# Optimization experiments

Measured on AMD Instinct MI355X. Metric: run time of the kernel, lower is better.

## Reference

```python
import jax, jax.numpy as jnp
from jax import lax
import numpy as np

N, C_IN, C_OUT, H, W, D = 16, 32, 64, 128, 128, 5


def setup_inputs() -> dict:
    key = jax.random.key(0)
    k1, k2, k3, k4 = jax.random.split(key, 4)
    x = jax.random.normal(k1, (N, 1, C_IN, H, W), jnp.float32)
    d = jax.random.normal(k2, (N, C_OUT, C_IN, D, D), jnp.float32)
    y = jax.random.normal(k3, (N, C_OUT, 1, H, W), jnp.float32)
    alpha = jax.random.uniform(k4, (N, 1, 1, 1), jnp.float32)
    return {"x": x, "d": d, "y": y, "alpha": alpha, "reg": 1.0}


def _cross_corr(wts, img, pad):
    # out[i, j, u, v] = sum_{h,w} wts[i,h,w] * img[j, h+u-pad, w+v-pad]
    # (valid sums, zero padding). Implements the per-sample full-image conv3d
    # of the torch code (cross-correlation, no kernel flip).
    out = lax.conv_general_dilated(img[:, None], wts[:, None], (1, 1),
                                   [(pad, pad), (pad, pad)])
    return out.transpose(1, 0, 2, 3)  # (Ci_wts, Cj_img, 2*pad+1, 2*pad+1)


def reference(x, d, y, alpha, reg):
    n, _, c_in, h, w = x.shape
    c_out, ds = d.shape[1], d.shape[-1]
    K = c_in * ds * ds
    # Full autocorrelation R[n,c0,c1,a,b] = sum x[c0,h,w]*x[c1,h+a-(ds-1), w+b-(ds-1)]
    R = jax.vmap(lambda xn: _cross_corr(xn, xn, ds - 1))(x[:, 0])  # (n,C,C,2ds-1,2ds-1)
    # Toeplitz block assembly: Q[(c0,p,q),(c1,s,t)] = R[c0,c1, s-p+ds-1, t-q+ds-1]
    shift = jnp.arange(ds)[None, :] - jnp.arange(ds)[:, None] + (ds - 1)  # [p,s]
    Qa = R[:, :, :, shift, :]            # (n,c0,c1,p,s,2ds-1)
    Qb = Qa[..., shift]                  # (n,c0,c1,p,s,q,t)
    Q = Qb.transpose(0, 1, 3, 5, 2, 4, 6).reshape(n, K, K)
    # X^T y: S[n,o,c,u,v] = sum y[o,h,w]*x[c, h+u-p0, w+v-p0], p0=(ds-1)//2
    S = jax.vmap(lambda yn, xn: _cross_corr(yn, xn, (ds - 1) // 2))(y[:, :, 0], x[:, 0])
    P = S.transpose(0, 2, 3, 4, 1).reshape(n, K, c_out)
    # Tikhonov regularization around previous dictionary d
    a = alpha.reshape(n, 1) * (h * w * reg / (ds * ds * c_in))  # (n,1)
    Q = Q + a[:, :, None] * jnp.eye(K, dtype=Q.dtype)
    P = P + a[:, :, None] * d.reshape(n, c_out, K).transpose(0, 2, 1)
    # Batched Cholesky solve: D = Q^{-1} P
    L = jnp.linalg.cholesky(Q)
    z = lax.linalg.triangular_solve(L, P, left_side=True, lower=True)
    Dsol = lax.linalg.triangular_solve(L, z, left_side=True, lower=True, transpose_a=True)
    return Dsol.reshape(n, c_in, ds, ds, c_out).transpose(0, 4, 1, 2, 3)
```

## Files before the change

kernel.cpp:

```cpp
#include <hip/hip_runtime.h>

#define R_SZ    737280
#define Q_SZ    10240000
#define P_SZ    819200
#define LI_SZ   1024000
#define W_SZ    4608000

typedef unsigned short u16;
typedef __attribute__((ext_vector_type(8))) short bf16x8;
typedef __attribute__((ext_vector_type(4))) float f32x4;

#define MFMA16(a, b, c) __builtin_amdgcn_mfma_f32_16x16x32_bf16(a, b, c, 0, 0, 0)

__device__ __forceinline__ float alpha_scale(const float* alpha, const float* reg, int n) {
  return alpha[n] * (16384.0f * reg[0] / 800.0f);
}

__device__ __forceinline__ u16 f2bf(float f) {
  union { float f; unsigned u; } v; v.f = f;
  unsigned r = v.u + 0x7FFFu + ((v.u >> 16) & 1u);
  return (u16)(r >> 16);
}
__device__ __forceinline__ float bf2f(u16 h) {
  union { unsigned u; float f; } v; v.u = ((unsigned)h) << 16; return v.f;
}

__device__ __forceinline__ bf16x8 load8(const u16* p) {
  union { uint4 d; bf16x8 v; } u;
  u.d = *(const uint4*)p;
  return u.v;
}

__device__ __forceinline__ bf16x8 build_frag(const unsigned* w, int s) {
  union { unsigned u[4]; bf16x8 v; } f;
  int b = s >> 1;
  if (s & 1) {
    #pragma unroll
    for (int k = 0; k < 4; ++k) f.u[k] = (w[b + k] >> 16) | (w[b + k + 1] << 16);
  } else {
    #pragma unroll
    for (int k = 0; k < 4; ++k) f.u[k] = w[b + k];
  }
  return f.v;
}

__device__ __forceinline__ void stage_row(u16* slot, int partStride,
                                          const float* __restrict__ img,
                                          int C, int r, bool valid,
                                          int tid, int nthr) {
  for (int idx = tid; idx < C * 16; idx += nthr) {
    int c = idx >> 4, m = idx & 15;
    float v[8];
    if (valid) {
      const float* p = img + ((size_t)c * 128 + r) * 128 + m * 8;
      float4 a = *(const float4*)p;
      float4 b = *(const float4*)(p + 4);
      v[0]=a.x; v[1]=a.y; v[2]=a.z; v[3]=a.w; v[4]=b.x; v[5]=b.y; v[6]=b.z; v[7]=b.w;
    } else {
      #pragma unroll
      for (int k = 0; k < 8; ++k) v[k] = 0.0f;
    }
    union { u16 s[8]; uint2 d[2]; } hh, ll;
    #pragma unroll
    for (int k = 0; k < 8; ++k) {
      u16 h = f2bf(v[k]);
      hh.s[k] = h;
      ll.s[k] = f2bf(v[k] - bf2f(h));
    }
    u16* dh = slot + c * 136 + 4 + m * 8;
    *(uint2*)(dh)     = hh.d[0];
    *(uint2*)(dh + 4) = hh.d[1];
    u16* dl = dh + partStride;
    *(uint2*)(dl)     = ll.d[0];
    *(uint2*)(dl + 4) = ll.d[1];
  }
}

#define SLOT_US 8704
#define PSTR_32 4352
#define YPSTR   8704

__global__ __launch_bounds__(640) void k_corrR_mfma(const float* __restrict__ x,
                                                    float* __restrict__ Rpart) {
  __shared__ __align__(16) u16 lds[5 * SLOT_US];
  int n  = blockIdx.x >> 4;
  int r0 = (blockIdx.x & 15) << 3;
  int tid = threadIdx.x;
  const float* xn = x + (size_t)n * 32 * 128 * 128;

  if (tid < 320) {
    int s = tid / 64, p = (tid >> 5) & 1, c = tid & 31;
    u16* b = lds + s * SLOT_US + p * PSTR_32 + c * 136;
    uint2 z; z.x = 0; z.y = 0;
    *(uint2*)b = z;
    *(uint2*)(b + 132) = z;
  }
  for (int rr = 0; rr < 5; ++rr) {
    int r = r0 + rr;
    stage_row(lds + (r % 5) * SLOT_US, PSTR_32, xn, 32, r, r < 128, tid, 640);
  }

  int wave = tid >> 6, lane = tid & 63;
  int du = wave >> 1, nt = wave & 1;
  int lm = lane & 15, q = lane >> 4;

  f32x4 acc[9][2];
  #pragma unroll
  for (int dvi = 0; dvi < 9; ++dvi)
    #pragma unroll
    for (int mt = 0; mt < 2; ++mt) acc[dvi][mt] = (f32x4){0.f, 0.f, 0.f, 0.f};

  for (int i = r0; i < r0 + 8; ++i) {
    __syncthreads();
    const u16* A  = lds + (i % 5) * SLOT_US;
    const u16* Bp = lds + ((i + du) % 5) * SLOT_US;
    #pragma unroll
    for (int ks = 0; ks < 4; ++ks) {
      int kb = ks * 32 + q * 8;
      bf16x8 af[2][2];
      #pragma unroll
      for (int pa = 0; pa < 2; ++pa)
        #pragma unroll
        for (int mt = 0; mt < 2; ++mt)
          af[pa][mt] = load8(A + pa * PSTR_32 + (mt * 16 + lm) * 136 + 4 + kb);
      #pragma unroll
      for (int pb = 0; pb < 2; ++pb) {
        const u16* wp = Bp + pb * PSTR_32 + (nt * 16 + lm) * 136 + kb;
        uint4 w0 = *(const uint4*)wp;
        uint4 w1 = *(const uint4*)(wp + 8);
        unsigned w[8] = {w0.x, w0.y, w0.z, w0.w, w1.x, w1.y, w1.z, w1.w};
        #pragma unroll
        for (int dvi = 0; dvi < 9; ++dvi) {
          bf16x8 bf = build_frag(w, dvi);
          #pragma unroll
          for (int mt = 0; mt < 2; ++mt)
            #pragma unroll
            for (int pa = 0; pa < 2; ++pa) {
              if (pa == 1 && pb == 1) continue;
              acc[dvi][mt] = MFMA16(af[pa][mt], bf, acc[dvi][mt]);
            }
        }
      }
    }
    __syncthreads();
    if (i + 1 < r0 + 8) {
      int r = i + 5;
      stage_row(lds + (r % 5) * SLOT_US, PSTR_32, xn, 32, r, r < 128, tid, 640);
    }
  }

  float* Rp = Rpart + (size_t)blockIdx.x * 46080;
  #pragma unroll
  for (int dvi = 0; dvi < 9; ++dvi)
    #pragma unroll
    for (int mt = 0; mt < 2; ++mt) {
      float* dst = Rp + (du * 9 + dvi) * 1024 + (nt * 16 + lm) * 32 + mt * 16 + q * 4;
      *(f32x4*)dst = acc[dvi][mt];
    }
}

__global__ void k_reduceR(const float* __restrict__ part, float* __restrict__ R) {
  int idx = blockIdx.x * 256 + threadIdx.x;
  int n = idx / 46080, rem = idx % 46080;
  const float* p = part + (size_t)n * 16 * 46080 + rem;
  float s = 0.0f;
  #pragma unroll
  for (int c = 0; c < 16; ++c) s += p[(size_t)c * 46080];
  R[idx] = s;
}

__global__ __launch_bounds__(640) void k_corrP_mfma(const float* __restrict__ x,
                                                    const float* __restrict__ y,
                                                    float* __restrict__ Ppart) {
  __shared__ __align__(16) u16 xs[5 * SLOT_US];
  __shared__ __align__(16) u16 ys[2 * YPSTR];
  int n  = blockIdx.x >> 4;
  int r0 = (blockIdx.x & 15) << 3;
  int tid = threadIdx.x;
  const float* xn = x + (size_t)n * 32 * 128 * 128;
  const float* yn = y + (size_t)n * 64 * 128 * 128;

  if (tid < 320) {
    int s = tid / 64, p = (tid >> 5) & 1, c = tid & 31;
    u16* b = xs + s * SLOT_US + p * PSTR_32 + c * 136;
    uint2 z; z.x = 0; z.y = 0;
    *(uint2*)b = z;
    *(uint2*)(b + 132) = z;
  }
  for (int rr = -2; rr <= 2; ++rr) {
    int r = r0 + rr;
    stage_row(xs + ((r + 10) % 5) * SLOT_US, PSTR_32, xn, 32, r,
              (r >= 0 && r < 128), tid, 640);
  }
  stage_row(ys, YPSTR, yn, 64, r0, true, tid, 640);

  int wave = tid >> 6, lane = tid & 63;
  int du = (wave >> 1) - 2, mh = wave & 1;
  int lm = lane & 15, q = lane >> 4;

  f32x4 acc[5][2][2];
  #pragma unroll
  for (int dvi = 0; dvi < 5; ++dvi)
    #pragma unroll
    for (int mt = 0; mt < 2; ++mt)
      #pragma unroll
      for (int nt = 0; nt < 2; ++nt)
        acc[dvi][mt][nt] = (f32x4){0.f, 0.f, 0.f, 0.f};

  for (int i = r0; i < r0 + 8; ++i) {
    __syncthreads();
    const u16* Bp = xs + ((i + du + 10) % 5) * SLOT_US;
    #pragma unroll
    for (int ks = 0; ks < 4; ++ks) {
      int kb = ks * 32 + q * 8;
      bf16x8 af[2][2];
      #pragma unroll
      for (int pa = 0; pa < 2; ++pa)
        #pragma unroll
        for (int mt = 0; mt < 2; ++mt)
          af[pa][mt] = load8(ys + pa * YPSTR + (mh * 32 + mt * 16 + lm) * 136 + 4 + kb);
      #pragma unroll
      for (int nt = 0; nt < 2; ++nt)
        #pragma unroll
        for (int pb = 0; pb < 2; ++pb) {
          const u16* wp = Bp + pb * PSTR_32 + (nt * 16 + lm) * 136 + kb;
          uint4 w0 = *(const uint4*)wp;
          uint4 w1 = *(const uint4*)(wp + 8);
          unsigned w[8] = {w0.x, w0.y, w0.z, w0.w, w1.x, w1.y, w1.z, w1.w};
          #pragma unroll
          for (int dvi = 0; dvi < 5; ++dvi) {
            bf16x8 bf = build_frag(w, dvi + 2);
            #pragma unroll
            for (int mt = 0; mt < 2; ++mt)
              #pragma unroll
              for (int pa = 0; pa < 2; ++pa) {
                if (pa == 1 && pb == 1) continue;
                acc[dvi][mt][nt] = MFMA16(af[pa][mt], bf, acc[dvi][mt][nt]);
              }
          }
        }
    }
    __syncthreads();
    if (i + 1 < r0 + 8) {
      int r = i + 3;
      stage_row(xs + ((r + 10) % 5) * SLOT_US, PSTR_32, xn, 32, r,
                (r >= 0 && r < 128), tid, 640);
      stage_row(ys, YPSTR, yn, 64, i + 1, true, tid, 640);
    }
  }

  float* Pp = Ppart + (size_t)blockIdx.x * 51200;
  #pragma unroll
  for (int dvi = 0; dvi < 5; ++dvi)
    #pragma unroll
    for (int mt = 0; mt < 2; ++mt)
      #pragma unroll
      for (int nt = 0; nt < 2; ++nt) {
        float* dst = Pp + ((du + 2) * 5 + dvi) * 2048 + (nt * 16 + lm) * 64
                        + mh * 32 + mt * 16 + q * 4;
        *(f32x4*)dst = acc[dvi][mt][nt];
      }
}

__global__ void k_reduceP(const float* __restrict__ part, const float* __restrict__ d,
                          const float* __restrict__ alpha, const float* __restrict__ reg,
                          float* __restrict__ P) {
  int idx = blockIdx.x * 256 + threadIdx.x;
  int n = idx / 51200, rem = idx % 51200;
  int k = rem >> 6, co = rem & 63;
  int ci = k / 25, ae = k % 25;
  const float* p = part + (size_t)n * 16 * 51200 + (ae * 32 + ci) * 64 + co;
  float s = 0.0f;
  #pragma unroll
  for (int c = 0; c < 16; ++c) s += p[(size_t)c * 51200];
  float a = alpha_scale(alpha, reg, n);
  P[idx] = s + a * d[((size_t)n * 64 + co) * 800 + k];
}

__global__ void k_buildQ(const float* __restrict__ R, float* __restrict__ Q,
                         const float* __restrict__ alpha, const float* __restrict__ reg) {
  int bid = blockIdx.x;
  int n = bid / 800, k1 = bid % 800;
  int c1 = k1 / 25, r1 = k1 % 25, a = r1 / 5, e = r1 % 5;
  float av = alpha_scale(alpha, reg, n);
  const float* Rn = R + (size_t)n * 45 * 1024;
  float* Qrow = Q + ((size_t)n * 800 + k1) * 800;
  for (int k2 = threadIdx.x; k2 < 800; k2 += 256) {
    int c2 = k2 / 25, r2 = k2 % 25, b = r2 / 5, f = r2 % 5;
    int du = b - a, dv = f - e;
    float v = (du >= 0)
      ? Rn[(du * 9 + dv + 4) * 1024 + c2 * 32 + c1]
      : Rn[((-du) * 9 + 4 - dv) * 1024 + c1 * 32 + c2];
    if (k2 == k1) v += av;
    Qrow[k2] = v;
  }
}

#define DS 82

__device__ void diag_factor_invert2(float* As, float* Bs,
                                    float* __restrict__ Ln, float* __restrict__ LnT,
                                    int tid) {
  __shared__ float Dinv_s[16 * 25];
  for (int s = 0; s < 16; ++s) {
    int b = 5 * s;
    float a[5][5], dinv[5];
    #pragma unroll
    for (int ii = 0; ii < 5; ++ii)
      #pragma unroll
      for (int kk = 0; kk <= ii; ++kk) a[ii][kk] = As[(b+ii)*DS + b+kk];
    #pragma unroll
    for (int jj = 0; jj < 5; ++jj) {
      float dd = sqrtf(a[jj][jj]);
      a[jj][jj] = dd; dinv[jj] = 1.0f / dd;
      #pragma unroll
      for (int ii = jj+1; ii < 5; ++ii) a[ii][jj] *= dinv[jj];
      #pragma unroll
      for (int ii = jj+1; ii < 5; ++ii)
        #pragma unroll
        for (int kk = jj+1; kk <= ii; ++kk) a[ii][kk] -= a[ii][jj] * a[kk][jj];
    }
    if (tid < 25) {
      int ii = tid / 5, kk = tid % 5;
      if (kk <= ii) As[(b+ii)*DS + b+kk] = a[ii][kk];
    }
    int m = 75 - b;
    for (int r = tid; r < m; r += 256) {
      int row = b + 5 + r;
      float w[5];
      #pragma unroll
      for (int c = 0; c < 5; ++c) {
        float av2 = As[row*DS + b + c];
        #pragma unroll
        for (int kk = 0; kk < c; ++kk) av2 -= w[kk] * a[c][kk];
        w[c] = av2 * dinv[c];
      }
      #pragma unroll
      for (int c = 0; c < 5; ++c) As[row*DS + b + c] = w[c];
    }
    __syncthreads();
    for (int idx = tid; idx < m*m; idx += 256) {
      int ii = idx / m, kk = idx % m;
      if (kk <= ii) {
        int ri = b+5+ii, rk = b+5+kk;
        float acc2 = As[ri*DS + rk];
        #pragma unroll
        for (int c = 0; c < 5; ++c) acc2 -= As[ri*DS + b+c] * As[rk*DS + b+c];
        As[ri*DS + rk] = acc2;
      }
    }
    __syncthreads();
  }

  if (tid < 16) {
    int i = tid;
    const float* Ab = As + (5*i)*DS + 5*i;
    float L5[5][5], Di[5][5];
    #pragma unroll
    for (int r = 0; r < 5; ++r)
      #pragma unroll
      for (int c = 0; c <= r; ++c) L5[r][c] = Ab[r*DS + c];
    #pragma unroll
    for (int c = 0; c < 5; ++c) {
      #pragma unroll
      for (int r = 0; r < c; ++r) Di[r][c] = 0.0f;
      Di[c][c] = 1.0f / L5[c][c];
      #pragma unroll
      for (int r = c+1; r < 5; ++r) {
        float sacc = 0.0f;
        #pragma unroll
        for (int k = c; k < r; ++k) sacc += L5[r][k] * Di[k][c];
        Di[r][c] = -sacc * (1.0f / L5[r][r]);
      }
    }
    #pragma unroll
    for (int r = 0; r < 5; ++r)
      #pragma unroll
      for (int c = 0; c < 5; ++c) Dinv_s[i*25 + r*5 + c] = Di[r][c];
  }
  __syncthreads();

  if (tid < 80) {
    int j = tid;
    for (int i = 0; i < 16; ++i) {
      float bv[5];
      #pragma unroll
      for (int r = 0; r < 5; ++r) bv[r] = (5*i + r == j) ? 1.0f : 0.0f;
      const float* Arow = As + (5*i)*DS;
      #pragma unroll 5
      for (int k = 0; k < 5*i; ++k) {
        float xc = Bs[k*DS + j];
        #pragma unroll
        for (int r = 0; r < 5; ++r) bv[r] -= Arow[r*DS + k] * xc;
      }
      #pragma unroll
      for (int r = 0; r < 5; ++r) {
        float v = 0.0f;
        #pragma unroll
        for (int c = 0; c <= r; ++c) v += Dinv_s[i*25 + r*5 + c] * bv[c];
        Bs[(5*i + r)*DS + j] = v;
      }
    }
  }
  __syncthreads();
  for (int idx = tid; idx < 6400; idx += 256) {
    int r = idx / 80, c = idx % 80;
    float v = (r >= c) ? Bs[r*DS + c] : 0.0f;
    Ln[idx] = v;
    LnT[c*80 + r] = v;
  }
}

__global__ __launch_bounds__(256) void k_diag0(const float* __restrict__ Q,
                                               float* __restrict__ Linv,
                                               float* __restrict__ LinvT) {
  __shared__ float As[80*DS];
  __shared__ float Bs[80*DS];
  int n = blockIdx.x, tid = threadIdx.x;
  const float* Qn = Q + (size_t)n * 640000;
  for (int idx = tid; idx < 6400; idx += 256) {
    int r = idx / 80, c = idx % 80;
    As[r*DS + c] = Qn[r*800 + c];
  }
  __syncthreads();
  diag_factor_invert2(As, Bs, Linv + (size_t)n*10*6400, LinvT + (size_t)n*10*6400, tid);
}

__global__ __launch_bounds__(256) void k_chol_step(float* __restrict__ Q,
                                                   float* __restrict__ Linv,
                                                   float* __restrict__ LinvT,
                                                   float* __restrict__ Wrm,
                                                   float* __restrict__ Wcm,
                                                   int t) {
  int nt = 9 - t;
  int T = nt * (nt + 1) / 2;
  int n = blockIdx.x / T;
  int rr = blockIdx.x % T;
  int i = 0;
  while (rr >= i + 1) { rr -= i + 1; ++i; }
  int j = rr;
  int bi = t + 1 + i, bj = t + 1 + j;

  __shared__ float Ls[80*DS];
  __shared__ float Aa[80*DS];
  __shared__ float W1[80*DS];
  __shared__ float W2[80*DS];
  int tid = threadIdx.x, tc = tid & 15, tr = tid >> 4;
  float* Qn = Q + (size_t)n * 640000;
  const float* Ln = Linv + ((size_t)n*10 + t) * 6400;

  for (int idx = tid; idx < 6400; idx += 256) {
    int r = idx / 80, c = idx % 80;
    Ls[r*DS + c] = Ln[idx];
    Aa[r*DS + c] = Qn[(size_t)(80*bi + r)*800 + 80*t + c];
  }
  __syncthreads();

  float acc[5][5];
  #pragma unroll
  for (int a = 0; a < 5; ++a)
    #pragma unroll
    for (int b = 0; b < 5; ++b) acc[a][b] = 0.0f;
  for (int k = 0; k < 80; ++k) {
    float av[5], bv[5];
    #pragma unroll
    for (int dd = 0; dd < 5; ++dd) { av[dd] = Aa[(5*tr+dd)*DS + k]; bv[dd] = Ls[(5*tc+dd)*DS + k]; }
    #pragma unroll
    for (int a = 0; a < 5; ++a)
      #pragma unroll
      for (int b = 0; b < 5; ++b) acc[a][b] += av[a] * bv[b];
  }
  #pragma unroll
  for (int a = 0; a < 5; ++a)
    #pragma unroll
    for (int b = 0; b < 5; ++b) W1[(5*tr+a)*DS + 5*tc+b] = acc[a][b];
  if (i == j) {
    int p = t*9 - t*(t-1)/2 + i;
    size_t base = ((size_t)n*45 + p) * 6400;
    #pragma unroll
    for (int a = 0; a < 5; ++a)
      #pragma unroll
      for (int b = 0; b < 5; ++b) {
        Wrm[base + (5*tr+a)*80 + 5*tc+b] = acc[a][b];
        Wcm[base + (5*tc+b)*80 + 5*tr+a] = acc[a][b];
      }
  }
  __syncthreads();

  const float* Wia = W1;
  const float* Wjb = W1;
  if (i != j) {
    for (int idx = tid; idx < 6400; idx += 256) {
      int r = idx / 80, c = idx % 80;
      Aa[r*DS + c] = Qn[(size_t)(80*bj + r)*800 + 80*t + c];
    }
    __syncthreads();
    #pragma unroll
    for (int a = 0; a < 5; ++a)
      #pragma unroll
      for (int b = 0; b < 5; ++b) acc[a][b] = 0.0f;
    for (int k = 0; k < 80; ++k) {
      float av[5], bv[5];
      #pragma unroll
      for (int dd = 0; dd < 5; ++dd) { av[dd] = Aa[(5*tr+dd)*DS + k]; bv[dd] = Ls[(5*tc+dd)*DS + k]; }
      #pragma unroll
      for (int a = 0; a < 5; ++a)
        #pragma unroll
        for (int b = 0; b < 5; ++b) acc[a][b] += av[a] * bv[b];
    }
    #pragma unroll
    for (int a = 0; a < 5; ++a)
      #pragma unroll
      for (int b = 0; b < 5; ++b) W2[(5*tr+a)*DS + 5*tc+b] = acc[a][b];
    Wjb = W2;
    __syncthreads();
  }

  for (int idx = tid; idx < 6400; idx += 256) {
    int r = idx / 80, c = idx % 80;
    Aa[r*DS + c] = Qn[(size_t)(80*bi + r)*800 + 80*bj + c];
  }
  __syncthreads();

  #pragma unroll
  for (int a = 0; a < 5; ++a)
    #pragma unroll
    for (int b = 0; b < 5; ++b) acc[a][b] = 0.0f;
  for (int k = 0; k < 80; ++k) {
    float av[5], bv[5];
    #pragma unroll
    for (int dd = 0; dd < 5; ++dd) { av[dd] = Wia[(5*tr+dd)*DS + k]; bv[dd] = Wjb[(5*tc+dd)*DS + k]; }
    #pragma unroll
    for (int a = 0; a < 5; ++a)
      #pragma unroll
      for (int b = 0; b < 5; ++b) acc[a][b] += av[a] * bv[b];
  }

  bool special = (i == 0 && j == 0);
  if (!special) {
    #pragma unroll
    for (int a = 0; a < 5; ++a)
      #pragma unroll
      for (int b = 0; b < 5; ++b)
        Qn[(size_t)(80*bi + 5*tr+a)*800 + 80*bj + 5*tc+b] =
          Aa[(5*tr+a)*DS + 5*tc+b] - acc[a][b];
  } else {
    #pragma unroll
    for (int a = 0; a < 5; ++a)
      #pragma unroll
      for (int b = 0; b < 5; ++b)
        Aa[(5*tr+a)*DS + 5*tc+b] -= acc[a][b];
    __syncthreads();
    diag_factor_invert2(Aa, Ls,
                        Linv  + ((size_t)n*10 + t + 1) * 6400,
                        LinvT + ((size_t)n*10 + t + 1) * 6400, tid);
  }
}

#define ZS 20

__device__ __forceinline__ void ldch8(float b[8], const float* __restrict__ Mp, int i) {
  #pragma unroll
  for (int q = 0; q < 8; ++q) b[q] = Mp[q * 80 + i];
}
__device__ __forceinline__ void mac8(const float b[8], const float* zp, int c0,
                                     float& a0, float& a1) {
  #pragma unroll
  for (int q = 0; q < 8; ++q) {
    float2 zv = *(const float2*)(zp + q * ZS + c0);
    a0 += b[q] * zv.x;
    a1 += b[q] * zv.y;
  }
}
__device__ __forceinline__ void seg80(const float* __restrict__ M, const float* zp,
                                      int i, int c0, float& a0, float& a1) {
  float A[8], B[8];
  ldch8(A, M, i);
  ldch8(B, M + 640, i);
  #pragma unroll
  for (int h = 0; h < 4; ++h) {
    mac8(A, zp + (16 * h) * ZS, c0, a0, a1);
    ldch8(A, M + (2 * h + 2) * 640, i);
    mac8(B, zp + (16 * h + 8) * ZS, c0, a0, a1);
    ldch8(B, M + (2 * h + 3) * 640, i);
  }
  mac8(A, zp + 64 * ZS, c0, a0, a1);
  mac8(B, zp + 72 * ZS, c0, a0, a1);
}

__global__ __launch_bounds__(640) void k_solve(const float* __restrict__ Linv,
                                               const float* __restrict__ LinvT,
                                               const float* __restrict__ Wrm,
                                               const float* __restrict__ Wcm,
                                               const float* __restrict__ P,
                                               float* __restrict__ out) {
  __shared__ float z[800 * ZS];
  int n = blockIdx.x >> 2;
  int qg = (blockIdx.x & 3) * 16;
  int tid = threadIdx.x;
  int i  = tid % 80;
  int c0 = (tid / 80) * 2;
  const float* Lb  = Linv  + (size_t)n * 10 * 6400;
  const float* LTb = LinvT + (size_t)n * 10 * 6400;
  const float* Wr  = Wrm + (size_t)n * 45 * 6400;
  const float* Wc  = Wcm + (size_t)n * 45 * 6400;

  for (int idx = tid; idx < 12800; idx += 640) {
    int k = idx >> 4, c = idx & 15;
    z[k * ZS + c] = P[((size_t)n * 800 + k) * 64 + qg + c];
  }

  for (int t = 0; t < 10; ++t) {
    __syncthreads();
    float a0 = 0.f, a1 = 0.f;
    seg80(LTb + t * 6400, &z[(80 * t) * ZS], i, c0, a0, a1);
    __syncthreads();
    *(float2*)&z[(80 * t + i) * ZS + c0] = make_float2(a0, a1);
    __syncthreads();
    int nseg = 9 - t;
    if (nseg > 0) {
      const float* Mc = Wc + (size_t)(t * 9 - t * (t - 1) / 2) * 6400;
      for (int s = 0; s < nseg; ++s) {
        float b0 = 0.f, b1 = 0.f;
        seg80(Mc + (size_t)s * 6400, &z[(80 * t) * ZS], i, c0, b0, b1);
        int u = t + 1 + s;
        float2* zp = (float2*)&z[(80 * u + i) * ZS + c0];
        float2 v = *zp; v.x -= b0; v.y -= b1; *zp = v;
      }
    }
  }

  for (int t = 9; t >= 0; --t) {
    __syncthreads();
    float a0 = 0.f, a1 = 0.f;
    seg80(Lb + t * 6400, &z[(80 * t) * ZS], i, c0, a0, a1);
    __syncthreads();
    *(float2*)&z[(80 * t + i) * ZS + c0] = make_float2(a0, a1);
    __syncthreads();
    for (int u = t - 1; u >= 0; --u) {
      int p = u * 9 - u * (u - 1) / 2 + (t - u - 1);
      float b0 = 0.f, b1 = 0.f;
      seg80(Wr + (size_t)p * 6400, &z[(80 * t) * ZS], i, c0, b0, b1);
      float2* zp = (float2*)&z[(80 * u + i) * ZS + c0];
      float2 v = *zp; v.x -= b0; v.y -= b1; *zp = v;
    }
  }

  __syncthreads();
  for (int idx = tid; idx < 12800; idx += 640) {
    int c = idx / 800, k = idx % 800;
    out[((size_t)n * 64 + qg + c) * 800 + k] = z[k * ZS + c];
  }
}

extern "C" void kernel_launch(void* const* d_in, const int* in_sizes, int n_in,
                              void* d_out, int out_size, void* d_ws, size_t ws_size,
                              hipStream_t stream) {
  const float* x     = (const float*)d_in[0];
  const float* d     = (const float*)d_in[1];
  const float* y     = (const float*)d_in[2];
  const float* alpha = (const float*)d_in[3];
  const float* reg   = (const float*)d_in[4];
  float* out = (float*)d_out;
  float* ws  = (float*)d_ws;

  float* R    = ws;
  float* Q    = R + R_SZ;
  float* P    = Q + Q_SZ;
  float* Li   = P + P_SZ;
  float* part = Li + LI_SZ;
  float* LiT  = part;
  float* Wrm  = part + LI_SZ;
  float* Wcm  = Wrm + W_SZ;

  k_corrR_mfma<<<256, 640, 0, stream>>>(x, part);
  k_reduceR<<<R_SZ / 256, 256, 0, stream>>>(part, R);
  k_corrP_mfma<<<256, 640, 0, stream>>>(x, y, part);
  k_reduceP<<<P_SZ / 256, 256, 0, stream>>>(part, d, alpha, reg, P);
  k_buildQ<<<16 * 800, 256, 0, stream>>>(R, Q, alpha, reg);

  k_diag0<<<16, 256, 0, stream>>>(Q, Li, LiT);
  for (int t = 0; t < 9; ++t) {
    int nt = 9 - t;
    k_chol_step<<<16 * nt * (nt + 1) / 2, 256, 0, stream>>>(Q, Li, LiT, Wrm, Wcm, t);
  }

  k_solve<<<64, 640, 0, stream>>>(Li, LiT, Wrm, Wcm, P, out);
}
```

Baseline: 1.500 ms.

## Restructure triangular solve: more blocks, register-cached z, row-major vector matrix loads

The solve kernel now launches 128 blocks of 320 threads instead of 64 blocks of 640, with each block handling 8 right-hand-side columns. Each z segment is copied from shared memory into 80 float2 registers per thread. Matrix rows are read as contiguous float4 loads by swapping in the transposed copies of Linv and W. The aim is to raise parallelism on the GPU and cut per-element LDS traffic, at the cost of heavy register pressure from the 80-entry cache, which may cause spills.

```diff
diff --git a/kernel.cpp b/kernel.cpp
--- a/kernel.cpp
+++ b/kernel.cpp
@@ -557,99 +557,114 @@
   }
 }
 
-#define ZS 20
-
-__device__ __forceinline__ void ldch8(float b[8], const float* __restrict__ Mp, int i) {
-  #pragma unroll
-  for (int q = 0; q < 8; ++q) b[q] = Mp[q * 80 + i];
-}
-__device__ __forceinline__ void mac8(const float b[8], const float* zp, int c0,
-                                     float& a0, float& a1) {
-  #pragma unroll
-  for (int q = 0; q < 8; ++q) {
-    float2 zv = *(const float2*)(zp + q * ZS + c0);
-    a0 += b[q] * zv.x;
-    a1 += b[q] * zv.y;
-  }
-}
-__device__ __forceinline__ void seg80(const float* __restrict__ M, const float* zp,
-                                      int i, int c0, float& a0, float& a1) {
-  float A[8], B[8];
-  ldch8(A, M, i);
-  ldch8(B, M + 640, i);
-  #pragma unroll
-  for (int h = 0; h < 4; ++h) {
-    mac8(A, zp + (16 * h) * ZS, c0, a0, a1);
-    ldch8(A, M + (2 * h + 2) * 640, i);
-    mac8(B, zp + (16 * h + 8) * ZS, c0, a0, a1);
-    ldch8(B, M + (2 * h + 3) * 640, i);
-  }
-  mac8(A, zp + 64 * ZS, c0, a0, a1);
-  mac8(B, zp + 72 * ZS, c0, a0, a1);
-}
-
-__global__ __launch_bounds__(640) void k_solve(const float* __restrict__ Linv,
-                                               const float* __restrict__ LinvT,
-                                               const float* __restrict__ Wrm,
-                                               const float* __restrict__ Wcm,
-                                               const float* __restrict__ P,
-                                               float* __restrict__ out) {
-  __shared__ float z[800 * ZS];
-  int n = blockIdx.x >> 2;
-  int qg = (blockIdx.x & 3) * 16;
+
+__device__ __forceinline__ void seg80c(const float* __restrict__ M, int i,
+                                       const float2 (&zc)[80],
+                                       float& a0, float& a1) {
+  const float* Mi = M + i * 80;
+  float4 A[8];
+  #pragma unroll
+  for (int q = 0; q < 8; ++q) A[q] = *(const float4*)(Mi + 4 * q);
+  #pragma unroll
+  for (int h = 0; h < 20; ++h) {
+    float4 v = A[h & 7];
+    if (h + 8 < 20) A[h & 7] = *(const float4*)(Mi + 4 * (h + 8));
+    a0 += v.x * zc[4*h].x;     a1 += v.x * zc[4*h].y;
+    a0 += v.y * zc[4*h + 1].x; a1 += v.y * zc[4*h + 1].y;
+    a0 += v.z * zc[4*h + 2].x; a1 += v.z * zc[4*h + 2].y;
+    a0 += v.w * zc[4*h + 3].x; a1 += v.w * zc[4*h + 3].y;
+  }
+}
+
+__global__ __launch_bounds__(320, 2) void k_solve(const float* __restrict__ Linv,
+                                                  const float* __restrict__ LinvT,
+                                                  const float* __restrict__ Wrm,
+                                                  const float* __restrict__ Wcm,
+                                                  const float* __restrict__ P,
+                                                  float* __restrict__ out) {
+  __shared__ __align__(16) float z2[4 * 800 * 2];
+  int n   = blockIdx.x >> 3;
+  int qg8 = (blockIdx.x & 7) << 3;
   int tid = threadIdx.x;
-  int i  = tid % 80;
-  int c0 = (tid / 80) * 2;
+  int i   = tid % 80;
+  int cp  = tid / 80;
   const float* Lb  = Linv  + (size_t)n * 10 * 6400;
   const float* LTb = LinvT + (size_t)n * 10 * 6400;
   const float* Wr  = Wrm + (size_t)n * 45 * 6400;
   const float* Wc  = Wcm + (size_t)n * 45 * 6400;
 
-  for (int idx = tid; idx < 12800; idx += 640) {
-    int k = idx >> 4, c = idx & 15;
-    z[k * ZS + c] = P[((size_t)n * 800 + k) * 64 + qg + c];
-  }
+  for (int idx = tid; idx < 6400; idx += 320) {
+    int k = idx >> 3, cc = idx & 7;
+    z2[((cc >> 1) * 800 + k) * 2 + (cc & 1)] =
+        P[((size_t)n * 800 + k) * 64 + qg8 + cc];
+  }
+
+  float2 zc[80];
 
   for (int t = 0; t < 10; ++t) {
     __syncthreads();
+    int zb = (cp * 800 + 80 * t) * 2;
+    #pragma unroll
+    for (int m = 0; m < 40; ++m) {
+      float4 v = *(const float4*)&z2[zb + 4 * m];
+      zc[2*m]     = make_float2(v.x, v.y);
+      zc[2*m + 1] = make_float2(v.z, v.w);
+    }
     float a0 = 0.f, a1 = 0.f;
-    seg80(LTb + t * 6400, &z[(80 * t) * ZS], i, c0, a0, a1);
-    __syncthreads();
-    *(float2*)&z[(80 * t + i) * ZS + c0] = make_float2(a0, a1);
-    __syncthreads();
+    seg80c(Lb + t * 6400, i, zc, a0, a1);
+    __syncthreads();
+    *(float2*)&z2[(cp * 800 + 80 * t + i) * 2] = make_float2(a0, a1);
+    __syncthreads();
+    #pragma unroll
+    for (int m = 0; m < 40; ++m) {
+      float4 v = *(const float4*)&z2[zb + 4 * m];
+      zc[2*m]     = make_float2(v.x, v.y);
+      zc[2*m + 1] = make_float2(v.z, v.w);
+    }
     int nseg = 9 - t;
-    if (nseg > 0) {
-      const float* Mc = Wc + (size_t)(t * 9 - t * (t - 1) / 2) * 6400;
-      for (int s = 0; s < nseg; ++s) {
-        float b0 = 0.f, b1 = 0.f;
-        seg80(Mc + (size_t)s * 6400, &z[(80 * t) * ZS], i, c0, b0, b1);
-        int u = t + 1 + s;
-        float2* zp = (float2*)&z[(80 * u + i) * ZS + c0];
-        float2 v = *zp; v.x -= b0; v.y -= b1; *zp = v;
-      }
+    const float* Mc = Wr + (size_t)(t * 9 - t * (t - 1) / 2) * 6400;
+    for (int s = 0; s < nseg; ++s) {
+      float b0 = 0.f, b1 = 0.f;
+      seg80c(Mc + (size_t)s * 6400, i, zc, b0, b1);
+      float2* zp = (float2*)&z2[(cp * 800 + 80 * (t + 1 + s) + i) * 2];
+      float2 v = *zp; v.x -= b0; v.y -= b1; *zp = v;
     }
   }
 
   for (int t = 9; t >= 0; --t) {
     __syncthreads();
+    int zb = (cp * 800 + 80 * t) * 2;
+    #pragma unroll
+    for (int m = 0; m < 40; ++m) {
+      float4 v = *(const float4*)&z2[zb + 4 * m];
+      zc[2*m]     = make_float2(v.x, v.y);
+      zc[2*m + 1] = make_float2(v.z, v.w);
+    }
     float a0 = 0.f, a1 = 0.f;
-    seg80(Lb + t * 6400, &z[(80 * t) * ZS], i, c0, a0, a1);
-    __syncthreads();
-    *(float2*)&z[(80 * t + i) * ZS + c0] = make_float2(a0, a1);
-    __syncthreads();
+    seg80c(LTb + t * 6400, i, zc, a0, a1);
+    __syncthreads();
+    *(float2*)&z2[(cp * 800 + 80 * t + i) * 2] = make_float2(a0, a1);
+    __syncthreads();
+    #pragma unroll
+    for (int m = 0; m < 40; ++m) {
+      float4 v = *(const float4*)&z2[zb + 4 * m];
+      zc[2*m]     = make_float2(v.x, v.y);
+      zc[2*m + 1] = make_float2(v.z, v.w);
+    }
     for (int u = t - 1; u >= 0; --u) {
       int p = u * 9 - u * (u - 1) / 2 + (t - u - 1);
       float b0 = 0.f, b1 = 0.f;
-      seg80(Wr + (size_t)p * 6400, &z[(80 * t) * ZS], i, c0, b0, b1);
-      float2* zp = (float2*)&z[(80 * u + i) * ZS + c0];
+      seg80c(Wc + (size_t)p * 6400, i, zc, b0, b1);
+      float2* zp = (float2*)&z2[(cp * 800 + 80 * u + i) * 2];
       float2 v = *zp; v.x -= b0; v.y -= b1; *zp = v;
     }
   }
 
   __syncthreads();
-  for (int idx = tid; idx < 12800; idx += 640) {
+  for (int idx = tid; idx < 6400; idx += 320) {
     int c = idx / 800, k = idx % 800;
-    out[((size_t)n * 64 + qg + c) * 800 + k] = z[k * ZS + c];
+    out[((size_t)n * 64 + qg8 + c) * 800 + k] =
+        z2[((c >> 1) * 800 + k) * 2 + (c & 1)];
   }
 }
 
@@ -685,5 +700,5 @@
     k_chol_step<<<16 * nt * (nt + 1) / 2, 256, 0, stream>>>(Q, Li, LiT, Wrm, Wcm, t);
   }
 
-  k_solve<<<64, 640, 0, stream>>>(Li, LiT, Wrm, Wcm, P, out);
-}
+  k_solve<<<16 * 8, 320, 0, stream>>>(Li, LiT, Wrm, Wcm, P, out);
+}
```

New measurement: 1.484 ms. Within noise of the previous version (-1.1%).
